# Kernel optimization log

Measured on AMD Instinct MI355X. Metric: run time of the kernel, lower is better.

## Reference

```python
import jax, jax.numpy as jnp
import numpy as np

N, L, C, K = 8, 6400, 256, 100  # batch, tokens per image (80x80), feat dim, n_topics
EPS = 1e-12  # F.normalize eps


def _l1_normalize(x):
    return x / jnp.maximum(jnp.sum(jnp.abs(x), axis=-1, keepdims=True), EPS)


def setup_inputs() -> dict:
    key = jax.random.key(0)
    k1, k2, k3 = jax.random.split(key, 3)
    feat = jax.random.normal(k1, (N, L, C), dtype=jnp.float32)
    prob_topics = jax.random.uniform(k2, (N, 2 * L, K), dtype=jnp.float32)
    # topics are hard (0/1) topic assignments per token
    topics = (jax.random.uniform(k3, (N, 2 * L, K)) > 0.5).astype(jnp.float32)
    return {"feat": feat, "prob_topics": prob_topics, "topics": topics, "n_samples": 8}


def reference(feat, prob_topics, topics, n_samples):
    n, l, c = feat.shape
    # ---- sample_topic (eval path: top-k over mixed topic distribution) ----
    p0, p1 = prob_topics[:, :l], prob_topics[:, l:]
    t0 = topics[:, :l]
    theta0 = _l1_normalize(jnp.sum(p0, axis=1))           # [N, K]
    theta1 = _l1_normalize(jnp.sum(p1, axis=1))           # [N, K]
    theta = _l1_normalize(theta0 * theta1)                # [N, K]
    _, sampled_inds = jax.lax.top_k(theta, n_samples)     # [N, n_samples]
    # gather topic columns for every token: [N, L, n_samples]
    sampled_topics0 = jnp.take_along_axis(t0, sampled_inds[:, None, :], axis=-1)
    topick = sampled_topics0[..., 0]                      # [N, L] binary membership of top topic

    # ---- reduce_feat: ragged boolean gather -> left-packed padded buffer ----
    # (padded to L, the static upper bound, for jit-compatible shapes)
    mask = topick > 0.5                                   # [N, L] selected tokens
    len_topic = jnp.sum(topick, axis=-1).astype(jnp.int32)  # [N]
    rank = jnp.cumsum(topick, axis=1).astype(jnp.int32) - 1  # dest slot per selected token
    dest = jnp.where(mask, rank, l)                       # unselected -> overflow slot l
    rows = jnp.arange(n)[:, None]                         # [N, 1]
    vals = jnp.where(mask[..., None], feat, 0.0)          # [N, L, C]
    resized_feat = jnp.zeros((n, l + 1, c), dtype=feat.dtype).at[rows, dest].set(vals)[:, :l]
    new_mask = jnp.arange(l)[None, :] < len_topic[:, None]  # [N, L] valid-slot mask
    return resized_feat, new_mask
```

## Files before the change

kernel.cpp:

```cpp
#include <hip/hip_runtime.h>

#define N 8
#define L 6400
#define C 256
#define K 100
#define CPS 32
#define RPC (L / CPS)

__global__ void kA_partial(const float* __restrict__ prob, double* __restrict__ P) {
    int b = blockIdx.x;
    int seg = b >> 5, chunk = b & 31;
    int t = threadIdx.x;
    int r8 = t >> 5, g = t & 31;
    const float4* base = (const float4*)prob
        + (size_t)seg * (L * 25) + (size_t)chunk * (RPC * 25);
    double a0 = 0, a1 = 0, a2 = 0, a3 = 0;
    if (g < 25) {
#pragma unroll
        for (int i = 0; i < RPC / 8; ++i) {
            float4 v = base[(i * 8 + r8) * 25 + g];
            a0 += v.x; a1 += v.y; a2 += v.z; a3 += v.w;
        }
    }
    __shared__ double sdata[8][100];
    if (g < 25) {
        int k4 = g * 4;
        sdata[r8][k4] = a0; sdata[r8][k4 + 1] = a1;
        sdata[r8][k4 + 2] = a2; sdata[r8][k4 + 3] = a3;
    }
    __syncthreads();
    if (t < 100) {
        double s = 0;
#pragma unroll
        for (int r = 0; r < 8; ++r) s += sdata[r][t];
        P[b * 100 + t] = s;
    }
}

__global__ void kB_argmax(const double* __restrict__ P, int* __restrict__ kstar) {
    int n = blockIdx.x, t = threadIdx.x;
    __shared__ double vbuf[100];
    if (t < 100) {
        const double* p0 = P + (size_t)(2 * n) * CPS * 100 + t;
        const double* p1 = P + (size_t)(2 * n + 1) * CPS * 100 + t;
        double s0 = 0, s1 = 0;
#pragma unroll 8
        for (int c = 0; c < CPS; ++c) { s0 += p0[c * 100]; s1 += p1[c * 100]; }
        vbuf[t] = s0 * s1;
    }
    __syncthreads();
    if (t == 0) {
        double best = -1.0; int bi = 0;
        for (int k = 0; k < K; ++k) {
            double v = vbuf[k];
            if (v > best) { best = v; bi = k; }
        }
        kstar[n] = bi;
    }
}

__global__ void kC_bits(const float* __restrict__ topics,
                        const int* __restrict__ kstar,
                        unsigned long long* __restrict__ bits) {
    int idx = blockIdx.x * 256 + threadIdx.x;
    int n = idx / L;
    int l = idx - n * L;
    int k = kstar[n];
    float v = topics[((size_t)n * 2 * L + (size_t)l) * K + (size_t)k];
    unsigned long long bal = __ballot(v > 0.5f);
    if ((threadIdx.x & 63) == 0) bits[idx >> 6] = bal;
}

__global__ void kD_scan(const unsigned long long* __restrict__ bits,
                        int* __restrict__ woffs, int* __restrict__ lenbuf,
                        float* __restrict__ out) {
    int n = blockIdx.x, t = threadIdx.x;
    __shared__ int cnts[100];
    __shared__ int len_s;
    if (t < 100) cnts[t] = __popcll(bits[n * 100 + t]);
    __syncthreads();
    if (t < 100) {
        int s = 0;
        for (int w = 0; w < t; ++w) s += cnts[w];
        woffs[n * 100 + t] = s;
    }
    if (t == 0) {
        int s = 0;
        for (int w = 0; w < 100; ++w) s += cnts[w];
        lenbuf[n] = s; len_s = s;
    }
    __syncthreads();
    int len = len_s;
    float* om = out + (size_t)N * L * C + (size_t)n * L;
    for (int idx = t; idx < L; idx += 128) om[idx] = (idx < len) ? 1.0f : 0.0f;
}

__global__ void __launch_bounds__(256)
kE_out(const float* __restrict__ feat,
       const unsigned long long* __restrict__ bits,
       const int* __restrict__ woffs, const int* __restrict__ lenbuf,
       float* __restrict__ out) {
    int r = blockIdx.x * 4 + (threadIdx.x >> 6);
    int lane = threadIdx.x & 63;
    int n = r / L;
    int l = r - n * L;
    unsigned long long word = bits[r >> 6];
    int len = lenbuf[n];
    const float4* f4 = (const float4*)feat;
    float4* o4 = (float4*)out;
    int bpos = l & 63;
    if ((word >> bpos) & 1ull) {
        int d = woffs[n * 100 + (l >> 6)]
              + __popcll(word & ((1ull << bpos) - 1ull));
        float4 v = f4[(size_t)r * 64 + lane];
        o4[((size_t)n * L + (size_t)d) * 64 + lane] = v;
    }
    if (l >= len)
        o4[(size_t)r * 64 + lane] = make_float4(0.f, 0.f, 0.f, 0.f);
}

extern "C" void kernel_launch(void* const* d_in, const int* in_sizes, int n_in,
                              void* d_out, int out_size, void* d_ws, size_t ws_size,
                              hipStream_t stream) {
    const float* feat   = (const float*)d_in[0];
    const float* prob   = (const float*)d_in[1];
    const float* topics = (const float*)d_in[2];

    double* P                 = (double*)d_ws;
    unsigned long long* bits  = (unsigned long long*)(P + 512 * 100);
    int* woffs                = (int*)(bits + 800);
    int* kstar                = woffs + 800;
    int* lenbuf               = kstar + 8;

    float* out = (float*)d_out;

    kA_partial<<<16 * CPS, 256, 0, stream>>>(prob, P);
    kB_argmax <<<N, 128, 0, stream>>>(P, kstar);
    kC_bits   <<<(N * L) / 256, 256, 0, stream>>>(topics, kstar, bits);
    kD_scan   <<<N, 128, 0, stream>>>(bits, woffs, lenbuf, out);
    kE_out    <<<(N * L) / 4, 256, 0, stream>>>(feat, bits, woffs, lenbuf, out);
}
```

Baseline: 170.4 us.

## Fuse argmax and scan into producer kernels via last-block atomic counters

Merges the small argmax and scan kernels into the preceding reduction and bit-building kernels. A global atomic counter lets the last block to finish do the follow-up work, and the mask output is now written inside the final gather kernel. This cuts launches from five to three plus a memset, removing per-launch gaps, but the finishing work is serialized in a single block and needs threadfence ordering.

```diff
diff --git a/kernel.cpp b/kernel.cpp
--- a/kernel.cpp
+++ b/kernel.cpp
@@ -6,8 +6,11 @@
 #define K 100
 #define CPS 32
 #define RPC (L / CPS)
+typedef unsigned long long u64;
 
-__global__ void kA_partial(const float* __restrict__ prob, double* __restrict__ P) {
+__global__ void __launch_bounds__(256)
+kern1(const float* __restrict__ prob, double* __restrict__ P,
+      int* __restrict__ kstar, unsigned int* __restrict__ ctr) {
     int b = blockIdx.x;
     int seg = b >> 5, chunk = b & 31;
     int t = threadIdx.x;
@@ -35,76 +38,78 @@
         for (int r = 0; r < 8; ++r) s += sdata[r][t];
         P[b * 100 + t] = s;
     }
-}
-
-__global__ void kB_argmax(const double* __restrict__ P, int* __restrict__ kstar) {
-    int n = blockIdx.x, t = threadIdx.x;
-    __shared__ double vbuf[100];
+    __syncthreads();
+    __shared__ unsigned int ord;
+    if (t == 0) { __threadfence(); ord = atomicAdd(ctr, 1); }
+    __syncthreads();
+    if (ord != 511) return;
+    __threadfence();
+    __shared__ double vbuf[8][100];
     if (t < 100) {
-        const double* p0 = P + (size_t)(2 * n) * CPS * 100 + t;
-        const double* p1 = P + (size_t)(2 * n + 1) * CPS * 100 + t;
-        double s0 = 0, s1 = 0;
+        for (int n = 0; n < N; ++n) {
+            const double* p0 = P + (size_t)(2 * n) * CPS * 100 + t;
+            const double* p1 = P + (size_t)(2 * n + 1) * CPS * 100 + t;
+            double s0 = 0, s1 = 0;
 #pragma unroll 8
-        for (int c = 0; c < CPS; ++c) { s0 += p0[c * 100]; s1 += p1[c * 100]; }
-        vbuf[t] = s0 * s1;
+            for (int c = 0; c < CPS; ++c) { s0 += p0[c * 100]; s1 += p1[c * 100]; }
+            vbuf[n][t] = s0 * s1;
+        }
     }
     __syncthreads();
-    if (t == 0) {
+    if (t < N) {
         double best = -1.0; int bi = 0;
         for (int k = 0; k < K; ++k) {
-            double v = vbuf[k];
+            double v = vbuf[t][k];
             if (v > best) { best = v; bi = k; }
         }
-        kstar[n] = bi;
+        kstar[t] = bi;
     }
 }
 
-__global__ void kC_bits(const float* __restrict__ topics,
-                        const int* __restrict__ kstar,
-                        unsigned long long* __restrict__ bits) {
+__global__ void __launch_bounds__(256)
+kern2(const float* __restrict__ topics, const int* __restrict__ kstar,
+      u64* __restrict__ bits, int* __restrict__ woffs,
+      int* __restrict__ lenbuf, unsigned int* __restrict__ ctr) {
     int idx = blockIdx.x * 256 + threadIdx.x;
     int n = idx / L;
     int l = idx - n * L;
     int k = kstar[n];
     float v = topics[((size_t)n * 2 * L + (size_t)l) * K + (size_t)k];
-    unsigned long long bal = __ballot(v > 0.5f);
+    u64 bal = __ballot(v > 0.5f);
     if ((threadIdx.x & 63) == 0) bits[idx >> 6] = bal;
-}
-
-__global__ void kD_scan(const unsigned long long* __restrict__ bits,
-                        int* __restrict__ woffs, int* __restrict__ lenbuf,
-                        float* __restrict__ out) {
-    int n = blockIdx.x, t = threadIdx.x;
-    __shared__ int cnts[100];
-    __shared__ int len_s;
-    if (t < 100) cnts[t] = __popcll(bits[n * 100 + t]);
     __syncthreads();
-    if (t < 100) {
+    __shared__ unsigned int ord;
+    if (threadIdx.x == 0) { __threadfence(); ord = atomicAdd(ctr, 1); }
+    __syncthreads();
+    if (ord != 199) return;
+    __threadfence();
+    __shared__ int cnts[N * 100];
+    int t = threadIdx.x;
+    for (int i = t; i < N * 100; i += 256) cnts[i] = __popcll(bits[i]);
+    __syncthreads();
+    if (t < N) {
         int s = 0;
-        for (int w = 0; w < t; ++w) s += cnts[w];
-        woffs[n * 100 + t] = s;
+        int* wo = woffs + t * 100;
+        const int* cn = cnts + t * 100;
+        for (int w = 0; w < 100; ++w) { wo[w] = s; s += cn[w]; }
+        lenbuf[t] = s;
     }
-    if (t == 0) {
-        int s = 0;
-        for (int w = 0; w < 100; ++w) s += cnts[w];
-        lenbuf[n] = s; len_s = s;
-    }
-    __syncthreads();
-    int len = len_s;
-    float* om = out + (size_t)N * L * C + (size_t)n * L;
-    for (int idx = t; idx < L; idx += 128) om[idx] = (idx < len) ? 1.0f : 0.0f;
 }
 
 __global__ void __launch_bounds__(256)
-kE_out(const float* __restrict__ feat,
-       const unsigned long long* __restrict__ bits,
-       const int* __restrict__ woffs, const int* __restrict__ lenbuf,
-       float* __restrict__ out) {
+kern3(const float* __restrict__ feat, const u64* __restrict__ bits,
+      const int* __restrict__ woffs, const int* __restrict__ lenbuf,
+      float* __restrict__ out) {
+    int gtid = blockIdx.x * 256 + threadIdx.x;
+    if (gtid < N * L) {
+        int nm = gtid / L;
+        out[(size_t)N * L * C + gtid] = ((gtid - nm * L) < lenbuf[nm]) ? 1.0f : 0.0f;
+    }
     int r = blockIdx.x * 4 + (threadIdx.x >> 6);
     int lane = threadIdx.x & 63;
     int n = r / L;
     int l = r - n * L;
-    unsigned long long word = bits[r >> 6];
+    u64 word = bits[r >> 6];
     int len = lenbuf[n];
     const float4* f4 = (const float4*)feat;
     float4* o4 = (float4*)out;
@@ -126,17 +131,17 @@
     const float* prob   = (const float*)d_in[1];
     const float* topics = (const float*)d_in[2];
 
-    double* P                 = (double*)d_ws;
-    unsigned long long* bits  = (unsigned long long*)(P + 512 * 100);
-    int* woffs                = (int*)(bits + 800);
-    int* kstar                = woffs + 800;
-    int* lenbuf               = kstar + 8;
+    double* P       = (double*)d_ws;
+    u64*    bits    = (u64*)(P + 512 * 100);
+    int*    woffs   = (int*)(bits + 800);
+    int*    kstar   = woffs + 800;
+    int*    lenbuf  = kstar + 8;
+    unsigned int* ctrs = (unsigned int*)(lenbuf + 8);
 
     float* out = (float*)d_out;
 
-    kA_partial<<<16 * CPS, 256, 0, stream>>>(prob, P);
-    kB_argmax <<<N, 128, 0, stream>>>(P, kstar);
-    kC_bits   <<<(N * L) / 256, 256, 0, stream>>>(topics, kstar, bits);
-    kD_scan   <<<N, 128, 0, stream>>>(bits, woffs, lenbuf, out);
-    kE_out    <<<(N * L) / 4, 256, 0, stream>>>(feat, bits, woffs, lenbuf, out);
+    hipMemsetAsync(ctrs, 0, 2 * sizeof(unsigned int), stream);
+    kern1<<<512,  256, 0, stream>>>(prob, P, kstar, ctrs + 0);
+    kern2<<<200,  256, 0, stream>>>(topics, kstar, bits, woffs, lenbuf, ctrs + 1);
+    kern3<<<12800, 256, 0, stream>>>(feat, bits, woffs, lenbuf, out);
 }
```

Measured after the change: 205.8 us. 1.21x slower.
